# Kernel tuning notes

Hardware: AMD Instinct MI355X
Metric: run time of the kernel (lower is better)

The kernel has to match this reference:

```python
import jax, jax.numpy as jnp
import numpy as np

K = 16  # kNN neighbors (global k in the original source)
# channel progression of the 6 DynamicEdgeConv layers
DIMS = [3, 32, 128, 256, 64, 32, 16]


def _knn_idx(x, k):
    # x: [B, N, D] -> indices of k nearest neighbors (incl. self), [B, N, k]
    sq = jnp.sum(x * x, axis=-1)                                   # [B, N]
    d = sq[:, :, None] + sq[:, None, :] - 2.0 * jnp.einsum('bnd,bmd->bnm', x, x)
    _, idx = jax.lax.top_k(-d, k)                                  # smallest distances
    return idx


def _edge_conv(x, W1, b1, W2, b2, k):
    # DynamicEdgeConv with mean aggregation: message = MLP([x_i, x_j - x_i])
    idx = _knn_idx(x, k)                                           # [B, N, k]
    xj = jax.vmap(lambda xb, ib: xb[ib])(x, idx)                   # [B, N, k, D]
    xi = jnp.broadcast_to(x[:, :, None, :], xj.shape)
    e = jnp.concatenate([xi, xj - xi], axis=-1)                    # [B, N, k, 2D]
    h = jax.nn.relu(e @ W1 + b1)
    h = jax.nn.relu(h @ W2 + b2)
    return jnp.mean(h, axis=2)                                     # [B, N, d_out]


def setup_inputs() -> dict:
    key = jax.random.key(0)
    ks = jax.random.split(key, 32)
    inp = {'x': jax.random.normal(ks[0], (8, 2048, 3), dtype=jnp.float32)}
    for l in range(6):
        din, dout = DIMS[l], DIMS[l + 1]
        s1 = 1.0 / np.sqrt(2 * din)
        s2 = 1.0 / np.sqrt(2 * dout)
        inp[f'W1_{l}'] = jax.random.normal(ks[1 + 4 * l], (2 * din, 2 * dout), dtype=jnp.float32) * s1
        inp[f'b1_{l}'] = jnp.zeros((2 * dout,), dtype=jnp.float32)
        inp[f'W2_{l}'] = jax.random.normal(ks[2 + 4 * l], (2 * dout, dout), dtype=jnp.float32) * s2
        inp[f'b2_{l}'] = jnp.zeros((dout,), dtype=jnp.float32)
    inp['Wf'] = jax.random.normal(ks[30], (16, 2), dtype=jnp.float32) * 0.25
    inp['bf'] = jnp.zeros((2,), dtype=jnp.float32)
    return inp


def reference(x, W1_0, b1_0, W2_0, b2_0, W1_1, b1_1, W2_1, b2_1,
              W1_2, b1_2, W2_2, b2_2, W1_3, b1_3, W2_3, b2_3,
              W1_4, b1_4, W2_4, b2_4, W1_5, b1_5, W2_5, b2_5, Wf, bf):
    params = [(W1_0, b1_0, W2_0, b2_0), (W1_1, b1_1, W2_1, b2_1),
              (W1_2, b1_2, W2_2, b2_2), (W1_3, b1_3, W2_3, b2_3),
              (W1_4, b1_4, W2_4, b2_4), (W1_5, b1_5, W2_5, b2_5)]
    for (W1, b1, W2, b2) in params:
        x = _edge_conv(x, W1, b1, W2, b2, K)
        x = jax.nn.relu(x)  # extra ReLU from forward (dropout is eval-mode identity)
    pooled = jnp.mean(x, axis=1)        # global_mean_pool over nodes -> [B, 16]
    return pooled @ Wf + bf             # [B, 2]
```

## Files before the change

### kernel.cpp

```cpp
#include <hip/hip_runtime.h>
#include <math.h>

#define NPTS 2048
#define NB 8
#define BN 16384
#define KNN 16

typedef _Float16 half4 __attribute__((ext_vector_type(4)));
typedef _Float16 half8 __attribute__((ext_vector_type(8)));
typedef float floatx16 __attribute__((ext_vector_type(16)));

__global__ __launch_bounds__(256) void sqprep_kernel(const float* __restrict__ X,
                                                     float* __restrict__ SQ,
                                                     const float* __restrict__ W1,
                                                     const float* __restrict__ b1,
                                                     float* __restrict__ Wcat,
                                                     float* __restrict__ bcat,
                                                     int din, int d2,
                                                     const float* __restrict__ W2,
                                                     _Float16* __restrict__ W2H,
                                                     _Float16* __restrict__ W2L,
                                                     int dout, int pb) {
    const int bid = blockIdx.x;
    if (bid < BN / 256) {
        int g = bid * 256 + threadIdx.x;
        const float* row = X + (size_t)g * din;
        float s = 0.f;
        for (int d = 0; d < din; ++d) s = fmaf(row[d], row[d], s);
        SQ[g] = s;
    } else if (bid < BN / 256 + pb) {
        int n4 = 2 * d2;
        int total = din * n4;
        int i = (bid - BN / 256) * 256 + threadIdx.x;
        if (i < total) {
            int d = i / n4, c = i - d * n4;
            float v;
            if (c < d2) v = W1[d * d2 + c] - W1[(din + d) * d2 + c];
            else        v = W1[(din + d) * d2 + (c - d2)];
            Wcat[i] = v;
        }
        if (i < n4) bcat[i] = (i < d2) ? b1[i] : 0.f;
    } else {
        int i = (bid - BN / 256 - pb) * 256 + threadIdx.x;
        if (i < d2 * dout) {
            int k = i / dout, c = i - k * dout;
            float wv = W2[i];
            _Float16 hv = (_Float16)wv;
            float rv = wv - (float)hv;
            W2H[(size_t)c * d2 + k] = hv;
            W2L[(size_t)c * d2 + k] = (_Float16)rv;
        }
    }
}

template <int DIN>
__global__ __launch_bounds__(256) void gram_kernel(const float* __restrict__ X,
                                                   const float* __restrict__ SQ,
                                                   float* __restrict__ DT) {
    __shared__ float As[32][132];
    __shared__ float Bs[32][132];
    const int t = threadIdx.x;
    const int tx = t & 15, ty = t >> 4;
    int bid = blockIdx.x;
    int bi = 0;
    while (bid >= 16 - bi) { bid -= 16 - bi; ++bi; }
    const int bj = bi + bid;
    const int i0 = bi * 128;
    const int j0 = bj * 128;
    const int z = blockIdx.z;
    const float* Xb = X + (size_t)z * NPTS * DIN;
    const float* SQb = SQ + (size_t)z * NPTS;
    float* DTb = DT + (size_t)z * NPTS * NPTS;

    const int e = t & 127;

    float acc[8][8];
    #pragma unroll
    for (int i = 0; i < 8; ++i)
        #pragma unroll
        for (int j = 0; j < 8; ++j) acc[i][j] = 0.f;

    if constexpr (DIN % 32 == 0) {
        const int rh = (t >> 7) * 16;
        const float* Ar = Xb + (size_t)(i0 + e) * DIN;
        const float* Br = Xb + (size_t)(j0 + e) * DIN;
        for (int k0 = 0; k0 < DIN; k0 += 32) {
            #pragma unroll
            for (int h = 0; h < 4; ++h) {
                float4 a = *(const float4*)(Ar + k0 + rh + h * 4);
                float4 b = *(const float4*)(Br + k0 + rh + h * 4);
                As[rh + h * 4 + 0][e] = a.x; As[rh + h * 4 + 1][e] = a.y;
                As[rh + h * 4 + 2][e] = a.z; As[rh + h * 4 + 3][e] = a.w;
                Bs[rh + h * 4 + 0][e] = b.x; Bs[rh + h * 4 + 1][e] = b.y;
                Bs[rh + h * 4 + 2][e] = b.z; Bs[rh + h * 4 + 3][e] = b.w;
            }
            __syncthreads();
            #pragma unroll
            for (int r = 0; r < 32; ++r) {
                float4 a0 = *(const float4*)&As[r][ty * 4];
                float4 a1 = *(const float4*)&As[r][64 + ty * 4];
                float4 b0 = *(const float4*)&Bs[r][tx * 4];
                float4 b1 = *(const float4*)&Bs[r][64 + tx * 4];
                float av[8] = {a0.x, a0.y, a0.z, a0.w, a1.x, a1.y, a1.z, a1.w};
                float bv[8] = {b0.x, b0.y, b0.z, b0.w, b1.x, b1.y, b1.z, b1.w};
                #pragma unroll
                for (int i = 0; i < 8; ++i)
                    #pragma unroll
                    for (int j = 0; j < 8; ++j)
                        acc[i][j] = fmaf(av[i], bv[j], acc[i][j]);
            }
            __syncthreads();
        }
    } else {
        const int rh = (t >> 7) * 8;
        #pragma unroll
        for (int i = 0; i < 8; ++i) {
            int k = rh + i;
            As[rh + i][e] = (k < DIN) ? Xb[(size_t)(i0 + e) * DIN + k] : 0.f;
            Bs[rh + i][e] = (k < DIN) ? Xb[(size_t)(j0 + e) * DIN + k] : 0.f;
        }
        __syncthreads();
        #pragma unroll
        for (int r = 0; r < 16; ++r) {
            float4 a0 = *(const float4*)&As[r][ty * 4];
            float4 a1 = *(const float4*)&As[r][64 + ty * 4];
            float4 b0 = *(const float4*)&Bs[r][tx * 4];
            float4 b1 = *(const float4*)&Bs[r][64 + tx * 4];
            float av[8] = {a0.x, a0.y, a0.z, a0.w, a1.x, a1.y, a1.z, a1.w};
            float bv[8] = {b0.x, b0.y, b0.z, b0.w, b1.x, b1.y, b1.z, b1.w};
            #pragma unroll
            for (int i = 0; i < 8; ++i)
                #pragma unroll
                for (int j = 0; j < 8; ++j)
                    acc[i][j] = fmaf(av[i], bv[j], acc[i][j]);
        }
        __syncthreads();
    }

    float sqi[8], sqj[8];
    #pragma unroll
    for (int i = 0; i < 8; ++i) {
        int ro = (i < 4) ? (ty * 4 + i) : (64 + ty * 4 + (i - 4));
        sqi[i] = SQb[i0 + ro];
    }
    #pragma unroll
    for (int j = 0; j < 8; ++j) {
        int co = (j < 4) ? (tx * 4 + j) : (64 + tx * 4 + (j - 4));
        sqj[j] = SQb[j0 + co];
    }
    #pragma unroll
    for (int i = 0; i < 8; ++i) {
        int ro = (i < 4) ? (ty * 4 + i) : (64 + ty * 4 + (i - 4));
        float* out = DTb + (size_t)(i0 + ro) * NPTS + j0;
        float4 o0, o1;
        o0.x = (sqi[i] + sqj[0]) - 2.f * acc[i][0];
        o0.y = (sqi[i] + sqj[1]) - 2.f * acc[i][1];
        o0.z = (sqi[i] + sqj[2]) - 2.f * acc[i][2];
        o0.w = (sqi[i] + sqj[3]) - 2.f * acc[i][3];
        o1.x = (sqi[i] + sqj[4]) - 2.f * acc[i][4];
        o1.y = (sqi[i] + sqj[5]) - 2.f * acc[i][5];
        o1.z = (sqi[i] + sqj[6]) - 2.f * acc[i][6];
        o1.w = (sqi[i] + sqj[7]) - 2.f * acc[i][7];
        *(float4*)(out + tx * 4) = o0;
        *(float4*)(out + 64 + tx * 4) = o1;
    }
    if (bi != bj) {
        #pragma unroll
        for (int j = 0; j < 8; ++j) {
            int co = (j < 4) ? (tx * 4 + j) : (64 + tx * 4 + (j - 4));
            float* out = DTb + (size_t)(j0 + co) * NPTS + i0;
            float4 o0, o1;
            o0.x = (sqi[0] + sqj[j]) - 2.f * acc[0][j];
            o0.y = (sqi[1] + sqj[j]) - 2.f * acc[1][j];
            o0.z = (sqi[2] + sqj[j]) - 2.f * acc[2][j];
            o0.w = (sqi[3] + sqj[j]) - 2.f * acc[3][j];
            o1.x = (sqi[4] + sqj[j]) - 2.f * acc[4][j];
            o1.y = (sqi[5] + sqj[j]) - 2.f * acc[5][j];
            o1.z = (sqi[6] + sqj[j]) - 2.f * acc[6][j];
            o1.w = (sqi[7] + sqj[j]) - 2.f * acc[7][j];
            *(float4*)(out + ty * 4) = o0;
            *(float4*)(out + 64 + ty * 4) = o1;
        }
    }
}

__global__ __launch_bounds__(256) void knn_select_kernel(const float* __restrict__ DT,
                                                         int* __restrict__ IDX, int qoff) {
    const int t = threadIdx.x;
    const int w = t >> 6, lane = t & 63;
    const int q = blockIdx.x * 4 + w;
    const float* dq = DT + (size_t)q * NPTS;
    const int l4 = lane << 2;

    float vals[32];
    #pragma unroll
    for (int s = 0; s < 8; ++s) {
        float4 v = *(const float4*)(dq + s * 256 + l4);
        vals[s * 4 + 0] = v.x; vals[s * 4 + 1] = v.y;
        vals[s * 4 + 2] = v.z; vals[s * 4 + 3] = v.w;
    }
    unsigned rm = 0;
    float best = INFINITY; int bslot = 32;
    #pragma unroll
    for (int sl = 0; sl < 32; ++sl)
        if (vals[sl] < best) { best = vals[sl]; bslot = sl; }

    for (int rep = 0; rep < KNN; ++rep) {
        int bj = (bslot < 32) ? ((bslot >> 2) * 256 + l4 + (bslot & 3)) : NPTS;
        float gb = best; int gj = bj;
        #pragma unroll
        for (int off = 1; off < 64; off <<= 1) {
            float ov = __shfl_xor(gb, off);
            int oj = __shfl_xor(gj, off);
            if (ov < gb || (ov == gb && oj < gj)) { gb = ov; gj = oj; }
        }
        if (lane == 0) IDX[(size_t)(qoff + q) * KNN + rep] = gj;
        if (((gj >> 2) & 63) == lane) {
            int slot = ((gj >> 8) << 2) | (gj & 3);
            rm |= (1u << slot);
            best = INFINITY; bslot = 32;
            #pragma unroll
            for (int sl = 0; sl < 32; ++sl)
                if (!(rm & (1u << sl)) && vals[sl] < best) { best = vals[sl]; bslot = sl; }
        }
    }
}

template <int KK, int NN>
__global__ __launch_bounds__(256) void gemm_big_kernel(const float* __restrict__ A,
                                                       const float* __restrict__ B,
                                                       const float* __restrict__ bias,
                                                       float* __restrict__ C) {
    __shared__ float As[32][132];
    __shared__ float Bs[32][132];
    const int t = threadIdx.x;
    const int tx = t & 15, ty = t >> 4;
    const int m0 = blockIdx.x * 128;
    const int c0 = blockIdx.y * 128;

    float acc[8][8];
    #pragma unroll
    for (int i = 0; i < 8; ++i)
        #pragma unroll
        for (int j = 0; j < 8; ++j) acc[i][j] = 0.f;

    const int e = t & 127;
    const int rh = (t >> 7) * 16;
    const float* Ar = A + (size_t)(m0 + e) * KK + rh;
    const int br = t & 31;
    const int bc = (t >> 5) * 16;
    const float* Wbase = B + (size_t)br * NN + c0 + bc;

    for (int k0 = 0; k0 < KK; k0 += 32) {
        #pragma unroll
        for (int h = 0; h < 4; ++h) {
            float4 a = *(const float4*)(Ar + k0 + h * 4);
            As[rh + h * 4 + 0][e] = a.x; As[rh + h * 4 + 1][e] = a.y;
            As[rh + h * 4 + 2][e] = a.z; As[rh + h * 4 + 3][e] = a.w;
            *(float4*)&Bs[br][bc + h * 4] = *(const float4*)(Wbase + (size_t)k0 * NN + h * 4);
        }
        __syncthreads();
        #pragma unroll
        for (int r = 0; r < 32; ++r) {
            float4 a0 = *(const float4*)&As[r][ty * 4];
            float4 a1 = *(const float4*)&As[r][64 + ty * 4];
            float4 b0 = *(const float4*)&Bs[r][tx * 4];
            float4 b1 = *(const float4*)&Bs[r][64 + tx * 4];
            float av[8] = {a0.x, a0.y, a0.z, a0.w, a1.x, a1.y, a1.z, a1.w};
            float bv[8] = {b0.x, b0.y, b0.z, b0.w, b1.x, b1.y, b1.z, b1.w};
            #pragma unroll
            for (int i = 0; i < 8; ++i)
                #pragma unroll
                for (int j = 0; j < 8; ++j)
                    acc[i][j] = fmaf(av[i], bv[j], acc[i][j]);
        }
        __syncthreads();
    }

    float bvv[8];
    #pragma unroll
    for (int j = 0; j < 8; ++j) {
        int co = (j < 4) ? (tx * 4 + j) : (64 + tx * 4 + (j - 4));
        bvv[j] = bias[c0 + co];
    }
    #pragma unroll
    for (int i = 0; i < 8; ++i) {
        int ro = (i < 4) ? (ty * 4 + i) : (64 + ty * 4 + (i - 4));
        float* out = C + (size_t)(m0 + ro) * NN + c0;
        float4 o0, o1;
        o0.x = acc[i][0] + bvv[0]; o0.y = acc[i][1] + bvv[1];
        o0.z = acc[i][2] + bvv[2]; o0.w = acc[i][3] + bvv[3];
        o1.x = acc[i][4] + bvv[4]; o1.y = acc[i][5] + bvv[5];
        o1.z = acc[i][6] + bvv[6]; o1.w = acc[i][7] + bvv[7];
        *(float4*)(out + tx * 4) = o0;
        *(float4*)(out + 64 + tx * 4) = o1;
    }
}

template <int KK, int NN>
__global__ __launch_bounds__(256) void gemm_pq_kernel(const float* __restrict__ A,
                                                      const float* __restrict__ B,
                                                      const float* __restrict__ bias,
                                                      float* __restrict__ C) {
    __shared__ float As[16][68];
    __shared__ float Bs[16][64];
    const int t = threadIdx.x;
    const int tx = t & 15, ty = t >> 4;
    const int m0 = blockIdx.x * 64;
    const int c0 = blockIdx.y * 64;
    float acc[4][4];
    #pragma unroll
    for (int i = 0; i < 4; ++i)
        #pragma unroll
        for (int j = 0; j < 4; ++j) acc[i][j] = 0.f;

    constexpr int KCH = (KK + 15) / 16;
    for (int kc = 0; kc < KCH; ++kc) {
        const int k0 = kc * 16;
        {
            int m = t & 63;
            int r4 = (t >> 6) * 4;
            if constexpr (KK % 16 == 0) {
                float4 v = *(const float4*)(A + (size_t)(m0 + m) * KK + k0 + r4);
                As[r4 + 0][m] = v.x; As[r4 + 1][m] = v.y;
                As[r4 + 2][m] = v.z; As[r4 + 3][m] = v.w;
            } else {
                #pragma unroll
                for (int i = 0; i < 4; ++i) {
                    int r = r4 + i;
                    As[r][m] = (k0 + r < KK) ? A[(size_t)(m0 + m) * KK + k0 + r] : 0.f;
                }
            }
        }
        {
            int r = t >> 4;
            int c = (t & 15) * 4;
            float4 v = make_float4(0.f, 0.f, 0.f, 0.f);
            if (k0 + r < KK) v = *(const float4*)(B + (size_t)(k0 + r) * NN + c0 + c);
            *(float4*)&Bs[r][c] = v;
        }
        __syncthreads();
        #pragma unroll
        for (int r = 0; r < 16; ++r) {
            float4 a4 = *(const float4*)&As[r][ty * 4];
            float4 b4 = *(const float4*)&Bs[r][tx * 4];
            float av[4] = {a4.x, a4.y, a4.z, a4.w};
            float bv[4] = {b4.x, b4.y, b4.z, b4.w};
            #pragma unroll
            for (int i = 0; i < 4; ++i)
                #pragma unroll
                for (int j = 0; j < 4; ++j)
                    acc[i][j] = fmaf(av[i], bv[j], acc[i][j]);
        }
        __syncthreads();
    }
    float4 bv4 = *(const float4*)(bias + c0 + tx * 4);
    float bv[4] = {bv4.x, bv4.y, bv4.z, bv4.w};
    #pragma unroll
    for (int i = 0; i < 4; ++i) {
        float4 o;
        o.x = acc[i][0] + bv[0];
        o.y = acc[i][1] + bv[1];
        o.z = acc[i][2] + bv[2];
        o.w = acc[i][3] + bv[3];
        *(float4*)(C + (size_t)(m0 + ty * 4 + i) * NN + c0 + tx * 4) = o;
    }
}

template <int D2, int DOUT>
__global__ __launch_bounds__(256) void edge_kernel(const float* __restrict__ PQ,
                                                   const int* __restrict__ IDX,
                                                   const float* __restrict__ W2,
                                                   const float* __restrict__ b2,
                                                   float* __restrict__ Xn) {
    constexpr int N4 = 2 * D2;
    __shared__ float As[16][68];
    __shared__ float Bs[16][64];
    __shared__ int gjs[64];
    const int t = threadIdx.x;
    const int tx = t & 15, ty = t >> 4;
    const int nb = blockIdx.x * 4;
    const int c0 = blockIdx.y * 64;

    if (t < 64) {
        int node = nb + (t >> 4);
        int bstart = (node / NPTS) * NPTS;
        gjs[t] = bstart + IDX[(size_t)node * KNN + (t & 15)];
    }
    __syncthreads();

    float acc[4][4];
    #pragma unroll
    for (int i = 0; i < 4; ++i)
        #pragma unroll
        for (int j = 0; j < 4; ++j) acc[i][j] = 0.f;

    const int e = t & 63;
    const int r4 = (t >> 6) * 4;
    const int gi = nb + (e >> 4);

    for (int k0 = 0; k0 < D2; k0 += 16) {
        {
            int gj = gjs[e];
            float4 p = *(const float4*)(PQ + (size_t)gi * N4 + k0 + r4);
            float4 q = *(const float4*)(PQ + (size_t)gj * N4 + D2 + k0 + r4);
            As[r4 + 0][e] = fmaxf(p.x + q.x, 0.f);
            As[r4 + 1][e] = fmaxf(p.y + q.y, 0.f);
            As[r4 + 2][e] = fmaxf(p.z + q.z, 0.f);
            As[r4 + 3][e] = fmaxf(p.w + q.w, 0.f);
        }
        {
            int r = t >> 4;
            int c = (t & 15) * 4;
            float4 v = make_float4(0.f, 0.f, 0.f, 0.f);
            if (c0 + c < DOUT) v = *(const float4*)(W2 + (size_t)(k0 + r) * DOUT + c0 + c);
            *(float4*)&Bs[r][c] = v;
        }
        __syncthreads();
        #pragma unroll
        for (int r = 0; r < 16; ++r) {
            float4 a4 = *(const float4*)&As[r][ty * 4];
            float4 b4 = *(const float4*)&Bs[r][tx * 4];
            float av[4] = {a4.x, a4.y, a4.z, a4.w};
            float bv[4] = {b4.x, b4.y, b4.z, b4.w};
            #pragma unroll
            for (int i = 0; i < 4; ++i)
                #pragma unroll
                for (int j = 0; j < 4; ++j)
                    acc[i][j] = fmaf(av[i], bv[j], acc[i][j]);
        }
        __syncthreads();
    }

    float bv[4];
    #pragma unroll
    for (int j = 0; j < 4; ++j) {
        int c = c0 + tx * 4 + j;
        bv[j] = (c < DOUT) ? b2[c] : 0.f;
    }
    float s[4];
    #pragma unroll
    for (int j = 0; j < 4; ++j) {
        float ss = 0.f;
        #pragma unroll
        for (int i = 0; i < 4; ++i) ss += fmaxf(acc[i][j] + bv[j], 0.f);
        s[j] = ss;
    }
    #pragma unroll
    for (int j = 0; j < 4; ++j) Bs[ty][tx * 4 + j] = s[j];
    __syncthreads();
    if ((ty & 3) == 0) {
        int node = nb + (ty >> 2);
        #pragma unroll
        for (int j = 0; j < 4; ++j) {
            int c = c0 + tx * 4 + j;
            if (c < DOUT) {
                int cc = tx * 4 + j;
                float tot = Bs[ty][cc] + Bs[ty + 1][cc] + Bs[ty + 2][cc] + Bs[ty + 3][cc];
                Xn[(size_t)node * DOUT + c] = tot * (1.f / 16.f);
            }
        }
    }
}

#define EBG_LOAD(KN)                                                                 \
  { _Pragma("unroll")                                                                \
    for (int h = 0; h < 4; ++h) {                                                    \
      pp[h] = *(const float4*)(Prow + (KN) + rh + h * 4);                            \
      qq[h] = *(const float4*)(Qrow + (KN) + rh + h * 4);                            \
    }                                                                                \
    wh = *(const half8*)(WHrow + (KN));                                              \
    wl = *(const half8*)(WLrow + (KN)); }

#define EBG_STAGE(dst)                                                               \
  { _Pragma("unroll")                                                                \
    for (int h = 0; h < 4; ++h) {                                                    \
      float a0 = fmaxf(pp[h].x + qq[h].x, 0.f);                                      \
      float a1 = fmaxf(pp[h].y + qq[h].y, 0.f);                                      \
      float a2 = fmaxf(pp[h].z + qq[h].z, 0.f);                                      \
      float a3 = fmaxf(pp[h].w + qq[h].w, 0.f);                                      \
      _Float16 h0 = (_Float16)a0, h1 = (_Float16)a1;                                 \
      _Float16 h2 = (_Float16)a2, h3 = (_Float16)a3;                                 \
      half4 hv, lv;                                                                  \
      hv.x = h0; hv.y = h1; hv.z = h2; hv.w = h3;                                    \
      lv.x = (_Float16)(a0 - (float)h0);                                             \
      lv.y = (_Float16)(a1 - (float)h1);                                             \
      lv.z = (_Float16)(a2 - (float)h2);                                             \
      lv.w = (_Float16)(a3 - (float)h3);                                             \
      *(half4*)&Ah[dst][e][rh + h * 4] = hv;                                         \
      *(half4*)&Al[dst][e][rh + h * 4] = lv;                                         \
    }                                                                                \
    *(half8*)&Bh[dst][eb][rb] = wh;                                                  \
    *(half8*)&Bl[dst][eb][rb] = wl; }

#define EBG_MFMA(cur)                                                                \
  { _Pragma("unroll")                                                                \
    for (int ks = 0; ks < 2; ++ks) {                                                 \
      const int kb = ks * 16 + lk;                                                   \
      half8 bf0  = *(const half8*)&Bh[cur][wc + lr][kb];                             \
      half8 blf0 = *(const half8*)&Bl[cur][wc + lr][kb];                             \
      half8 bf1  = *(const half8*)&Bh[cur][wc + 32 + lr][kb];                        \
      half8 blf1 = *(const half8*)&Bl[cur][wc + 32 + lr][kb];                        \
      _Pragma("unroll")                                                              \
      for (int i = 0; i < 2; ++i) {                                                  \
        half8 af  = *(const half8*)&Ah[cur][wr + i * 32 + lr][kb];                   \
        half8 alf = *(const half8*)&Al[cur][wr + i * 32 + lr][kb];                   \
        acc[i][0] = __builtin_amdgcn_mfma_f32_32x32x16_f16(af,  bf0,  acc[i][0], 0, 0, 0); \
        acc[i][0] = __builtin_amdgcn_mfma_f32_32x32x16_f16(af,  blf0, acc[i][0], 0, 0, 0); \
        acc[i][0] = __builtin_amdgcn_mfma_f32_32x32x16_f16(alf, bf0,  acc[i][0], 0, 0, 0); \
        acc[i][1] = __builtin_amdgcn_mfma_f32_32x32x16_f16(af,  bf1,  acc[i][1], 0, 0, 0); \
        acc[i][1] = __builtin_amdgcn_mfma_f32_32x32x16_f16(af,  blf1, acc[i][1], 0, 0, 0); \
        acc[i][1] = __builtin_amdgcn_mfma_f32_32x32x16_f16(alf, bf1,  acc[i][1], 0, 0, 0); \
      }                                                                              \
    } }

template <int D2, int DOUT>
__global__ __launch_bounds__(512) void edge_big_mfma_kernel(const float* __restrict__ PQ,
                                                            const int* __restrict__ IDX,
                                                            const _Float16* __restrict__ W2H,
                                                            const _Float16* __restrict__ W2L,
                                                            const float* __restrict__ b2,
                                                            float* __restrict__ Xn) {
    constexpr int N4 = 2 * D2;
    constexpr int NSTEP = D2 / 32;
    __shared__ _Float16 Ah[2][256][40];
    __shared__ _Float16 Al[2][256][40];
    __shared__ _Float16 Bh[2][128][40];
    __shared__ _Float16 Bl[2][128][40];
    __shared__ int gjs[256];
    const int t = threadIdx.x;
    const int nb16 = blockIdx.x * 16;
    const int c0 = blockIdx.y * 128;

    if (t < 256) {
        int node = nb16 + (t >> 4);
        int bstart = (node / NPTS) * NPTS;
        gjs[t] = bstart + IDX[(size_t)node * KNN + (t & 15)];
    }
    __syncthreads();

    const int e  = t & 255;
    const int rh = (t >> 8) * 16;
    const int gi = nb16 + (e >> 4);
    const int gj = gjs[e];
    const float* Prow = PQ + (size_t)gi * N4;
    const float* Qrow = PQ + (size_t)gj * N4 + D2;
    const int eb = t & 127;
    const int rb = (t >> 7) * 8;
    const _Float16* WHrow = W2H + (size_t)(c0 + eb) * D2 + rb;
    const _Float16* WLrow = W2L + (size_t)(c0 + eb) * D2 + rb;

    const int w = t >> 6;
    const int lane = t & 63;
    const int wr = (w >> 1) * 64;
    const int wc = (w & 1) * 64;
    const int lr = lane & 31;
    const int lk = (lane >> 5) * 8;
    const int hsel = lane >> 5;

    floatx16 acc[2][2];
    #pragma unroll
    for (int i = 0; i < 2; ++i)
        #pragma unroll
        for (int j = 0; j < 2; ++j)
            #pragma unroll
            for (int r = 0; r < 16; ++r) acc[i][j][r] = 0.f;

    float4 pp[4], qq[4];
    half8 wh, wl;

    EBG_LOAD(0)
    EBG_STAGE(0)
    EBG_LOAD(32)
    asm volatile("s_waitcnt lgkmcnt(0)" ::: "memory");
    __builtin_amdgcn_s_barrier();
    asm volatile("" ::: "memory");

    for (int s = 0; s < NSTEP - 1; ++s) {
        const int cur = s & 1;
        EBG_MFMA(cur)
        EBG_STAGE(cur ^ 1)
        const int kn = (s + 2 < NSTEP) ? (s + 2) * 32 : (NSTEP - 1) * 32;
        EBG_LOAD(kn)
        asm volatile("s_waitcnt lgkmcnt(0)" ::: "memory");
        __builtin_amdgcn_s_barrier();
        asm volatile("" ::: "memory");
    }
    EBG_MFMA((NSTEP - 1) & 1)

    float bb[2];
    bb[0] = b2[c0 + wc + lr];
    bb[1] = b2[c0 + wc + 32 + lr];
    #pragma unroll
    for (int i = 0; i < 2; ++i) {
        int node0 = nb16 + ((wr + i * 32) >> 4);
        #pragma unroll
        for (int j = 0; j < 2; ++j) {
            float sA = 0.f, sB = 0.f;
            #pragma unroll
            for (int r = 0; r < 8; ++r)  sA += fmaxf(acc[i][j][r] + bb[j], 0.f);
            #pragma unroll
            for (int r = 8; r < 16; ++r) sB += fmaxf(acc[i][j][r] + bb[j], 0.f);
            sA += __shfl_xor(sA, 32);
            sB += __shfl_xor(sB, 32);
            if (hsel == 0) {
                int col = c0 + wc + j * 32 + lr;
                Xn[(size_t)node0 * DOUT + col] = sA * (1.f / 16.f);
                Xn[(size_t)(node0 + 1) * DOUT + col] = sB * (1.f / 16.f);
            }
        }
    }
}
#undef EBG_LOAD
#undef EBG_STAGE
#undef EBG_MFMA

#define EM_STAGE_MFMA(KC, QQ, POK, KP)                                               \
  {                                                                                  \
    half8 wh0 = *(const half8*)(WHrow + (KC));                                       \
    half8 wl0 = *(const half8*)(WLrow + (KC));                                       \
    _Pragma("unroll")                                                                \
    for (int h = 0; h < 4; ++h) {                                                    \
      float4 p = *(const float4*)(Prow + (KC) + rh + h * 4);                         \
      float a0 = fmaxf(p.x + QQ[h].x, 0.f);                                          \
      float a1 = fmaxf(p.y + QQ[h].y, 0.f);                                          \
      float a2 = fmaxf(p.z + QQ[h].z, 0.f);                                          \
      float a3 = fmaxf(p.w + QQ[h].w, 0.f);                                          \
      _Float16 h0 = (_Float16)a0, h1 = (_Float16)a1;                                 \
      _Float16 h2 = (_Float16)a2, h3 = (_Float16)a3;                                 \
      half4 hv, lv;                                                                  \
      hv.x = h0; hv.y = h1; hv.z = h2; hv.w = h3;                                    \
      lv.x = (_Float16)(a0 - (float)h0);                                             \
      lv.y = (_Float16)(a1 - (float)h1);                                             \
      lv.z = (_Float16)(a2 - (float)h2);                                             \
      lv.w = (_Float16)(a3 - (float)h3);                                             \
      *(half4*)&Ah[e][rh + h * 4] = hv;                                              \
      *(half4*)&Al[e][rh + h * 4] = lv;                                              \
    }                                                                                \
    *(half8*)&Bh[wrB][wkB] = wh0;                                                    \
    *(half8*)&Bl[wrB][wkB] = wl0;                                                    \
    if (POK) {                                                                       \
      _Pragma("unroll")                                                              \
      for (int h = 0; h < 4; ++h)                                                    \
        QQ[h] = *(const float4*)(Qrow + (KP) + rh + h * 4);                          \
    }                                                                                \
    asm volatile("s_waitcnt lgkmcnt(0)" ::: "memory");                               \
    __builtin_amdgcn_s_barrier();                                                    \
    asm volatile("" ::: "memory");                                                   \
    _Pragma("unroll")                                                                \
    for (int ks = 0; ks < 2; ++ks) {                                                 \
      const int kb = ks * 16 + lk;                                                   \
      half8 bf0 = *(const half8*)&Bh[wc + lr][kb];                                   \
      half8 blf0 = *(const half8*)&Bl[wc + lr][kb];                                  \
      _Pragma("unroll")                                                              \
      for (int i = 0; i < 2; ++i) {                                                  \
        half8 af = *(const half8*)&Ah[wr + i * 32 + lr][kb];                         \
        half8 alf = *(const half8*)&Al[wr + i * 32 + lr][kb];                        \
        acc[i] = __builtin_amdgcn_mfma_f32_32x32x16_f16(af, bf0, acc[i], 0, 0, 0);   \
        acc[i] = __builtin_amdgcn_mfma_f32_32x32x16_f16(af, blf0, acc[i], 0, 0, 0);  \
        acc[i] = __builtin_amdgcn_mfma_f32_32x32x16_f16(alf, bf0, acc[i], 0, 0, 0);  \
      }                                                                              \
    }                                                                                \
    asm volatile("" ::: "memory");                                                   \
    __builtin_amdgcn_s_barrier();                                                    \
    asm volatile("" ::: "memory");                                                   \
  }

template <int D2, int DOUT>
__global__ __launch_bounds__(256) void edge_mid_mfma_kernel(const float* __restrict__ PQ,
                                                            const int* __restrict__ IDX,
                                                            const _Float16* __restrict__ W2H,
                                                            const _Float16* __restrict__ W2L,
                                                            const float* __restrict__ b2,
                                                            float* __restrict__ Xn) {
    constexpr int N4 = 2 * D2;
    __shared__ _Float16 Ah[128][40];
    __shared__ _Float16 Al[128][40];
    __shared__ _Float16 Bh[64][40];
    __shared__ _Float16 Bl[64][40];
    __shared__ int gjs[128];
    const int t = threadIdx.x;
    const int nb8 = blockIdx.x * 8;

    if (t < 128) {
        int node = nb8 + (t >> 4);
        int bstart = (node / NPTS) * NPTS;
        gjs[t] = bstart + IDX[(size_t)node * KNN + (t & 15)];
    }
    __syncthreads();

    const int e = t & 127;
    const int rh = (t >> 7) * 16;
    const int gi = nb8 + (e >> 4);
    const int gj = gjs[e];
    const float* Prow = PQ + (size_t)gi * N4;
    const float* Qrow = PQ + (size_t)gj * N4 + D2;
    const int wrB = t & 63;
    const int wkB = (t >> 6) * 8;
    const _Float16* WHrow = W2H + (size_t)wrB * D2 + wkB;
    const _Float16* WLrow = W2L + (size_t)wrB * D2 + wkB;

    const int w = t >> 6;
    const int lane = t & 63;
    const int wr = (w >> 1) * 64;
    const int wc = (w & 1) * 32;
    const int lr = lane & 31;
    const int lk = (lane >> 5) * 8;
    const int hsel = lane >> 5;

    floatx16 acc[2];
    #pragma unroll
    for (int i = 0; i < 2; ++i)
        #pragma unroll
        for (int r = 0; r < 16; ++r) acc[i][r] = 0.f;

    float4 qqA[4], qqB[4];
    #pragma unroll
    for (int h = 0; h < 4; ++h) qqA[h] = *(const float4*)(Qrow + rh + h * 4);
    #pragma unroll
    for (int h = 0; h < 4; ++h) qqB[h] = *(const float4*)(Qrow + 32 + rh + h * 4);

    for (int k0 = 0; k0 < D2; k0 += 64) {
        EM_STAGE_MFMA(k0,      qqA, (k0 + 64 < D2), k0 + 64)
        EM_STAGE_MFMA(k0 + 32, qqB, (k0 + 96 < D2), k0 + 96)
    }

    float bb = b2[wc + lr];
    #pragma unroll
    for (int i = 0; i < 2; ++i) {
        int node0 = nb8 + ((wr + i * 32) >> 4);
        float sA = 0.f, sB = 0.f;
        #pragma unroll
        for (int r = 0; r < 8; ++r)  sA += fmaxf(acc[i][r] + bb, 0.f);
        #pragma unroll
        for (int r = 8; r < 16; ++r) sB += fmaxf(acc[i][r] + bb, 0.f);
        sA += __shfl_xor(sA, 32);
        sB += __shfl_xor(sB, 32);
        if (hsel == 0) {
            int col = wc + lr;
            Xn[(size_t)node0 * DOUT + col] = sA * (1.f / 16.f);
            Xn[(size_t)(node0 + 1) * DOUT + col] = sB * (1.f / 16.f);
        }
    }
}
#undef EM_STAGE_MFMA

__global__ __launch_bounds__(256) void final_kernel(const float* __restrict__ X,
                                                    const float* __restrict__ Wf,
                                                    const float* __restrict__ bfin,
                                                    float* __restrict__ out) {
    __shared__ float red[16][17];
    __shared__ float pool[16];
    const int b = blockIdx.x;
    const int t = threadIdx.x;
    const int c = t & 15, rg = t >> 4;
    float s = 0.f;
    for (int n = rg; n < NPTS; n += 16) s += X[(size_t)(b * NPTS + n) * 16 + c];
    red[rg][c] = s;
    __syncthreads();
    if (t < 16) {
        float tot = 0.f;
        #pragma unroll
        for (int i = 0; i < 16; ++i) tot += red[i][t];
        pool[t] = tot * (1.f / NPTS);
    }
    __syncthreads();
    if (t < 2) {
        float a = bfin[t];
        #pragma unroll
        for (int cc = 0; cc < 16; ++cc) a = fmaf(pool[cc], Wf[cc * 2 + t], a);
        out[b * 2 + t] = a;
    }
}

template <int DIN, int DOUT>
static void run_layer(const float* Xin, float* Xout, float* PQ, float* SQ, int* IDX,
                      float* WCAT, float* BCAT, _Float16* W2H, _Float16* W2L,
                      const float* W1, const float* b1, const float* W2, const float* b2,
                      hipStream_t stream) {
    constexpr int D2 = 2 * DOUT;
    constexpr int N4 = 2 * D2;
    constexpr int prep_blocks = (DIN * N4 + 255) / 256;
    constexpr int w2_blocks = (DOUT >= 64) ? ((D2 * DOUT + 255) / 256) : 0;
    sqprep_kernel<<<BN / 256 + prep_blocks + w2_blocks, 256, 0, stream>>>(
        Xin, SQ, W1, b1, WCAT, BCAT, DIN, D2, W2, W2H, W2L,
        (DOUT >= 64) ? DOUT : 0, prep_blocks);
    for (int h = 0; h < 2; ++h) {
        dim3 gg(136, 1, 4);
        gram_kernel<DIN><<<gg, 256, 0, stream>>>(Xin + (size_t)h * 4 * NPTS * DIN,
                                                 SQ + (size_t)h * 4 * NPTS, PQ);
        knn_select_kernel<<<2048, 256, 0, stream>>>(PQ, IDX, h * 8192);
    }
    if constexpr (N4 % 128 == 0 && DIN % 32 == 0) {
        dim3 g1(BN / 128, N4 / 128);
        gemm_big_kernel<DIN, N4><<<g1, 256, 0, stream>>>(Xin, WCAT, BCAT, PQ);
    } else {
        dim3 g1(BN / 64, N4 / 64);
        gemm_pq_kernel<DIN, N4><<<g1, 256, 0, stream>>>(Xin, WCAT, BCAT, PQ);
    }
    if constexpr (DOUT >= 128) {
        dim3 g2(BN / 16, DOUT / 128);
        edge_big_mfma_kernel<D2, DOUT><<<g2, 512, 0, stream>>>(PQ, IDX, W2H, W2L, b2, Xout);
    } else if constexpr (DOUT == 64) {
        dim3 g2(BN / 8, 1);
        edge_mid_mfma_kernel<D2, DOUT><<<g2, 256, 0, stream>>>(PQ, IDX, W2H, W2L, b2, Xout);
    } else {
        dim3 g2(BN / 4, (DOUT + 63) / 64);
        edge_kernel<D2, DOUT><<<g2, 256, 0, stream>>>(PQ, IDX, W2, b2, Xout);
    }
}

extern "C" void kernel_launch(void* const* d_in, const int* in_sizes, int n_in,
                              void* d_out, int out_size, void* d_ws, size_t ws_size,
                              hipStream_t stream) {
    (void)in_sizes; (void)n_in; (void)out_size; (void)ws_size;
    const float* x = (const float*)d_in[0];
    const float* W1a[6]; const float* b1a[6]; const float* W2a[6]; const float* b2a[6];
    for (int l = 0; l < 6; ++l) {
        W1a[l] = (const float*)d_in[1 + 4 * l];
        b1a[l] = (const float*)d_in[2 + 4 * l];
        W2a[l] = (const float*)d_in[3 + 4 * l];
        b2a[l] = (const float*)d_in[4 + 4 * l];
    }
    const float* Wf = (const float*)d_in[25];
    const float* bfin = (const float*)d_in[26];

    float* ws = (float*)d_ws;
    float* X0   = ws;
    float* X1   = X0 + (size_t)BN * 256;
    float* PQ   = X1 + (size_t)BN * 256;
    float* SQ   = PQ + (size_t)BN * 1024;
    int*   IDX  = (int*)(SQ + BN);
    float* WCAT = (float*)(IDX + (size_t)BN * KNN);
    float* BCAT = WCAT + 131072;
    _Float16* W2H = (_Float16*)(BCAT + 1024);
    _Float16* W2L = W2H + 131072;

    run_layer<3,   32>(x,  X0, PQ, SQ, IDX, WCAT, BCAT, W2H, W2L, W1a[0], b1a[0], W2a[0], b2a[0], stream);
    run_layer<32, 128>(X0, X1, PQ, SQ, IDX, WCAT, BCAT, W2H, W2L, W1a[1], b1a[1], W2a[1], b2a[1], stream);
    run_layer<128,256>(X1, X0, PQ, SQ, IDX, WCAT, BCAT, W2H, W2L, W1a[2], b1a[2], W2a[2], b2a[2], stream);
    run_layer<256, 64>(X0, X1, PQ, SQ, IDX, WCAT, BCAT, W2H, W2L, W1a[3], b1a[3], W2a[3], b2a[3], stream);
    run_layer<64,  32>(X1, X0, PQ, SQ, IDX, WCAT, BCAT, W2H, W2L, W1a[4], b1a[4], W2a[4], b2a[4], stream);
    run_layer<32,  16>(X0, X1, PQ, SQ, IDX, WCAT, BCAT, W2H, W2L, W1a[5], b1a[5], W2a[5], b2a[5], stream);
    final_kernel<<<NB, 256, 0, stream>>>(X1, Wf, bfin, (float*)d_out);
}
```

Baseline: 1.845 ms.

## Compute kNN Gram matrix with split-fp16 MFMA for wide layers

For layers whose input width is a multiple of 32, the pairwise-distance Gram matrix is now computed on MFMA units. Each fp32 value is split into fp16 high and low parts, and three MFMA products are accumulated to approximate fp32 precision. This replaces the scalar FMA path. The new kernel computes all 256 tiles instead of exploiting symmetry over 136 tiles, and its output stores are less vectorized. The approximation could also change neighbor ordering on near-ties.

```diff
diff --git a/kernel.cpp b/kernel.cpp
--- a/kernel.cpp
+++ b/kernel.cpp
@@ -80,38 +80,7 @@
         #pragma unroll
         for (int j = 0; j < 8; ++j) acc[i][j] = 0.f;
 
-    if constexpr (DIN % 32 == 0) {
-        const int rh = (t >> 7) * 16;
-        const float* Ar = Xb + (size_t)(i0 + e) * DIN;
-        const float* Br = Xb + (size_t)(j0 + e) * DIN;
-        for (int k0 = 0; k0 < DIN; k0 += 32) {
-            #pragma unroll
-            for (int h = 0; h < 4; ++h) {
-                float4 a = *(const float4*)(Ar + k0 + rh + h * 4);
-                float4 b = *(const float4*)(Br + k0 + rh + h * 4);
-                As[rh + h * 4 + 0][e] = a.x; As[rh + h * 4 + 1][e] = a.y;
-                As[rh + h * 4 + 2][e] = a.z; As[rh + h * 4 + 3][e] = a.w;
-                Bs[rh + h * 4 + 0][e] = b.x; Bs[rh + h * 4 + 1][e] = b.y;
-                Bs[rh + h * 4 + 2][e] = b.z; Bs[rh + h * 4 + 3][e] = b.w;
-            }
-            __syncthreads();
-            #pragma unroll
-            for (int r = 0; r < 32; ++r) {
-                float4 a0 = *(const float4*)&As[r][ty * 4];
-                float4 a1 = *(const float4*)&As[r][64 + ty * 4];
-                float4 b0 = *(const float4*)&Bs[r][tx * 4];
-                float4 b1 = *(const float4*)&Bs[r][64 + tx * 4];
-                float av[8] = {a0.x, a0.y, a0.z, a0.w, a1.x, a1.y, a1.z, a1.w};
-                float bv[8] = {b0.x, b0.y, b0.z, b0.w, b1.x, b1.y, b1.z, b1.w};
-                #pragma unroll
-                for (int i = 0; i < 8; ++i)
-                    #pragma unroll
-                    for (int j = 0; j < 8; ++j)
-                        acc[i][j] = fmaf(av[i], bv[j], acc[i][j]);
-            }
-            __syncthreads();
-        }
-    } else {
+    {
         const int rh = (t >> 7) * 8;
         #pragma unroll
         for (int i = 0; i < 8; ++i) {
@@ -180,6 +149,105 @@
             o1.w = (sqi[7] + sqj[j]) - 2.f * acc[7][j];
             *(float4*)(out + ty * 4) = o0;
             *(float4*)(out + 64 + ty * 4) = o1;
+        }
+    }
+}
+
+template <int DIN>
+__global__ __launch_bounds__(256) void gram_mfma_kernel(const float* __restrict__ X,
+                                                        const float* __restrict__ SQ,
+                                                        float* __restrict__ DT) {
+    __shared__ _Float16 Ah[128][40];
+    __shared__ _Float16 Al[128][40];
+    __shared__ _Float16 Bh[128][40];
+    __shared__ _Float16 Bl[128][40];
+    const int t = threadIdx.x;
+    const int bi = blockIdx.x >> 4, bj = blockIdx.x & 15;
+    const int i0 = bi * 128, j0 = bj * 128;
+    const int z = blockIdx.z;
+    const float* Xb = X + (size_t)z * NPTS * DIN;
+    const float* SQb = SQ + (size_t)z * NPTS;
+    float* DTb = DT + (size_t)z * NPTS * NPTS;
+
+    const int e = t & 127;
+    const int rh = (t >> 7) * 16;
+    const float* Ar = Xb + (size_t)(i0 + e) * DIN + rh;
+    const float* Br = Xb + (size_t)(j0 + e) * DIN + rh;
+
+    const int w = t >> 6;
+    const int lane = t & 63;
+    const int wr = (w >> 1) * 64;
+    const int wc = (w & 1) * 64;
+    const int lr = lane & 31;
+    const int lk = (lane >> 5) * 8;
+    const int hsel = lane >> 5;
+
+    floatx16 acc[2][2];
+    #pragma unroll
+    for (int i = 0; i < 2; ++i)
+        #pragma unroll
+        for (int j = 0; j < 2; ++j)
+            #pragma unroll
+            for (int r = 0; r < 16; ++r) acc[i][j][r] = 0.f;
+
+    for (int k0 = 0; k0 < DIN; k0 += 32) {
+        #pragma unroll
+        for (int h = 0; h < 4; ++h) {
+            float4 a = *(const float4*)(Ar + k0 + h * 4);
+            float4 b = *(const float4*)(Br + k0 + h * 4);
+            _Float16 ah0 = (_Float16)a.x, ah1 = (_Float16)a.y, ah2 = (_Float16)a.z, ah3 = (_Float16)a.w;
+            half4 av, alv;
+            av.x = ah0; av.y = ah1; av.z = ah2; av.w = ah3;
+            alv.x = (_Float16)(a.x - (float)ah0);
+            alv.y = (_Float16)(a.y - (float)ah1);
+            alv.z = (_Float16)(a.z - (float)ah2);
+            alv.w = (_Float16)(a.w - (float)ah3);
+            *(half4*)&Ah[e][rh + h * 4] = av;
+            *(half4*)&Al[e][rh + h * 4] = alv;
+            _Float16 bh0 = (_Float16)b.x, bh1 = (_Float16)b.y, bh2 = (_Float16)b.z, bh3 = (_Float16)b.w;
+            half4 bv, blv;
+            bv.x = bh0; bv.y = bh1; bv.z = bh2; bv.w = bh3;
+            blv.x = (_Float16)(b.x - (float)bh0);
+            blv.y = (_Float16)(b.y - (float)bh1);
+            blv.z = (_Float16)(b.z - (float)bh2);
+            blv.w = (_Float16)(b.w - (float)bh3);
+            *(half4*)&Bh[e][rh + h * 4] = bv;
+            *(half4*)&Bl[e][rh + h * 4] = blv;
+        }
+        __syncthreads();
+        #pragma unroll
+        for (int ks = 0; ks < 2; ++ks) {
+            const int kb = ks * 16 + lk;
+            half8 bf0  = *(const half8*)&Bh[wc + lr][kb];
+            half8 blf0 = *(const half8*)&Bl[wc + lr][kb];
+            half8 bf1  = *(const half8*)&Bh[wc + 32 + lr][kb];
+            half8 blf1 = *(const half8*)&Bl[wc + 32 + lr][kb];
+            #pragma unroll
+            for (int i = 0; i < 2; ++i) {
+                half8 af  = *(const half8*)&Ah[wr + i * 32 + lr][kb];
+                half8 alf = *(const half8*)&Al[wr + i * 32 + lr][kb];
+                acc[i][0] = __builtin_amdgcn_mfma_f32_32x32x16_f16(af,  bf0,  acc[i][0], 0, 0, 0);
+                acc[i][0] = __builtin_amdgcn_mfma_f32_32x32x16_f16(af,  blf0, acc[i][0], 0, 0, 0);
+                acc[i][0] = __builtin_amdgcn_mfma_f32_32x32x16_f16(alf, bf0,  acc[i][0], 0, 0, 0);
+                acc[i][1] = __builtin_amdgcn_mfma_f32_32x32x16_f16(af,  bf1,  acc[i][1], 0, 0, 0);
+                acc[i][1] = __builtin_amdgcn_mfma_f32_32x32x16_f16(af,  blf1, acc[i][1], 0, 0, 0);
+                acc[i][1] = __builtin_amdgcn_mfma_f32_32x32x16_f16(alf, bf1,  acc[i][1], 0, 0, 0);
+            }
+        }
+        __syncthreads();
+    }
+
+    const float sqj0 = SQb[j0 + wc + lr];
+    const float sqj1 = SQb[j0 + wc + 32 + lr];
+    #pragma unroll
+    for (int i = 0; i < 2; ++i) {
+        #pragma unroll
+        for (int r = 0; r < 16; ++r) {
+            const int row = wr + i * 32 + (r & 3) + 8 * (r >> 2) + 4 * hsel;
+            const float sqi = SQb[i0 + row];
+            float* out = DTb + (size_t)(i0 + row) * NPTS + j0 + wc;
+            out[lr]      = (sqi + sqj0) - 2.f * acc[i][0][r];
+            out[32 + lr] = (sqi + sqj1) - 2.f * acc[i][1][r];
         }
     }
 }
@@ -786,9 +854,15 @@
         Xin, SQ, W1, b1, WCAT, BCAT, DIN, D2, W2, W2H, W2L,
         (DOUT >= 64) ? DOUT : 0, prep_blocks);
     for (int h = 0; h < 2; ++h) {
-        dim3 gg(136, 1, 4);
-        gram_kernel<DIN><<<gg, 256, 0, stream>>>(Xin + (size_t)h * 4 * NPTS * DIN,
-                                                 SQ + (size_t)h * 4 * NPTS, PQ);
+        if constexpr (DIN % 32 == 0) {
+            dim3 gg(256, 1, 4);
+            gram_mfma_kernel<DIN><<<gg, 256, 0, stream>>>(Xin + (size_t)h * 4 * NPTS * DIN,
+                                                          SQ + (size_t)h * 4 * NPTS, PQ);
+        } else {
+            dim3 gg(136, 1, 4);
+            gram_kernel<DIN><<<gg, 256, 0, stream>>>(Xin + (size_t)h * 4 * NPTS * DIN,
+                                                     SQ + (size_t)h * 4 * NPTS, PQ);
+        }
         knn_select_kernel<<<2048, 256, 0, stream>>>(PQ, IDX, h * 8192);
     }
     if constexpr (N4 % 128 == 0 && DIN % 32 == 0) {
```

Result: faster. 1.726 ms, median of 2 (-6.5%).
